# Kernel tuning notes

Hardware: AMD Instinct MI355X
Metric: run time of the kernel (lower is better)

Reference implementation:

```python
import jax, jax.numpy as jnp
import numpy as np

LN_EPS = 1e-6

def layernorm(x, scale, bias):
    mu = jnp.mean(x, axis=-1, keepdims=True)
    var = jnp.mean(jnp.square(x - mu), axis=-1, keepdims=True)
    return (x - mu) * jax.lax.rsqrt(var + LN_EPS) * scale + bias

def setup_inputs() -> dict:
    key = jax.random.key(0)
    ks = jax.random.split(key, 8)
    B, S, Dm = 2, 2048, 1024
    H, Dh, E, De = 16, 64, 8, 1024
    s = 0.02
    return {
        'x': jax.random.normal(ks[0], (B, S, Dm), jnp.float32),
        'ln1_scale': jnp.ones((Dm,), jnp.float32),
        'ln1_bias': jnp.zeros((Dm,), jnp.float32),
        'Wqkv': jax.random.normal(ks[1], (Dm, 3 * H * Dh), jnp.float32) * s,
        'bqkv': jnp.zeros((3 * H * Dh,), jnp.float32),
        'Wo': jax.random.normal(ks[2], (H * Dh, Dm), jnp.float32) * s,
        'bo': jnp.zeros((Dm,), jnp.float32),
        'ln2_scale': jnp.ones((Dm,), jnp.float32),
        'ln2_bias': jnp.zeros((Dm,), jnp.float32),
        'router_W': jax.random.normal(ks[3], (Dm, E), jnp.float32) * s,
        'We': jax.random.normal(ks[4], (E, Dm, De), jnp.float32) * s,
        'be': jnp.zeros((E, De), jnp.float32),
        'Wmo': jax.random.normal(ks[5], (De, Dm), jnp.float32) * s,
        'bmo': jnp.zeros((Dm,), jnp.float32),
    }

def reference(x, ln1_scale, ln1_bias, Wqkv, bqkv, Wo, bo,
              ln2_scale, ln2_bias, router_W, We, be, Wmo, bmo):
    B, S, Dm = x.shape
    H, Dh = 16, 64
    # ---- attention sublayer ----
    y = layernorm(x, ln1_scale, ln1_bias)
    qkv = (y @ Wqkv + bqkv).reshape(B, S, 3, H, Dh)
    qkv = jnp.transpose(qkv, (2, 0, 3, 1, 4))  # [3,B,H,S,Dh]
    q, k, v = qkv[0], qkv[1], qkv[2]
    scale = 1.0 / jnp.sqrt(jnp.float32(Dh))
    attn = jax.nn.softmax(jnp.einsum('bhsd,bhtd->bhst', q, k) * scale, axis=-1)
    o = jnp.einsum('bhst,bhtd->bhsd', attn, v)
    o = jnp.transpose(o, (0, 2, 1, 3)).reshape(B, S, H * Dh)
    x = x + (o @ Wo + bo)
    # ---- dense soft-MoE sublayer ----
    y = layernorm(x, ln2_scale, ln2_bias)
    routing = jax.nn.softmax(jnp.einsum('bsh,he->bse', y, router_W), axis=-1)
    expert_out = jnp.einsum('bsh,ehf->bsef', y, We) + be  # [B,S,E,De]
    combined = jnp.einsum('bse,bsef->bsf', routing, expert_out)
    x = x + (combined @ Wmo + bmo)
    return x
```

## Files before the change

### kernel.cpp

```cpp
#include <hip/hip_runtime.h>
#include <hip/hip_bf16.h>

typedef unsigned short u16;
typedef float f32x4 __attribute__((ext_vector_type(4)));
typedef short s16x8 __attribute__((ext_vector_type(8)));
typedef unsigned short u16x4 __attribute__((ext_vector_type(4)));
typedef unsigned short u16x8 __attribute__((ext_vector_type(8)));

#define T_TOK 4096
#define DM 1024
#define NQKV 3072
#define LN_EPS 1e-6f
#define KDIM 1024
#define NT 32

__device__ __forceinline__ void gll16(const void* g, void* l) {
    __builtin_amdgcn_global_load_lds(
        (const __attribute__((address_space(1))) void*)g,
        (__attribute__((address_space(3))) void*)l, 16, 0, 0);
}

__device__ __forceinline__ void xcd_swz(int& bx, int& by) {
    const int gx = gridDim.x, gy = gridDim.y;
    const int nwg = gx * gy;
    const int lin = by * gx + bx;
    const int cpx = nwg >> 3;
    const int swz = (lin & 7) * cpx + (lin >> 3);
    bx = swz % gx;
    by = swz / gx;
}

__device__ __forceinline__ void bf16_split(float x, u16& hi, u16& lo) {
    unsigned xb = __float_as_uint(x);
    unsigned rh = xb + 0x7fffu + ((xb >> 16) & 1u);
    hi = (u16)(rh >> 16);
    float hf = __uint_as_float(((unsigned)hi) << 16);
    float rs = x - hf;
    unsigned rb = __float_as_uint(rs);
    unsigned rl = rb + 0x7fffu + ((rb >> 16) & 1u);
    lo = (u16)(rl >> 16);
}
__device__ __forceinline__ float bf16_comb(u16 h, u16 l) {
    return __uint_as_float(((unsigned)h) << 16) + __uint_as_float(((unsigned)l) << 16);
}

#define MFMA3(ACC, AH, AL, BH, BL) { \
    ACC = __builtin_amdgcn_mfma_f32_16x16x32_bf16(AH, BH, ACC, 0, 0, 0); \
    ACC = __builtin_amdgcn_mfma_f32_16x16x32_bf16(AH, BL, ACC, 0, 0, 0); \
    ACC = __builtin_amdgcn_mfma_f32_16x16x32_bf16(AL, BH, ACC, 0, 0, 0); }

__global__ __launch_bounds__(256)
void convert_w(const float* __restrict__ src, u16* __restrict__ dh,
               u16* __restrict__ dl, int K, int N) {
    const int e = blockIdx.z;
    src += (size_t)e * K * N;
    dh  += (size_t)e * K * N;
    dl  += (size_t)e * K * N;
    __shared__ float ts[64][65];
    const int t = threadIdx.x;
    const int k0 = blockIdx.y * 64, n0 = blockIdx.x * 64;
    const int r = t >> 4, c4 = (t & 15) * 4;
    #pragma unroll
    for (int i = 0; i < 4; ++i) {
        const int kr = r + i * 16;
        float4 v = *(const float4*)(src + (size_t)(k0 + kr) * N + n0 + c4);
        ts[kr][c4 + 0] = v.x; ts[kr][c4 + 1] = v.y;
        ts[kr][c4 + 2] = v.z; ts[kr][c4 + 3] = v.w;
    }
    __syncthreads();
    #pragma unroll
    for (int i = 0; i < 4; ++i) {
        const int nr = r + i * 16;
        u16x4 h4, l4;
        #pragma unroll
        for (int j = 0; j < 4; ++j) {
            u16 h, l; bf16_split(ts[c4 + j][nr], h, l);
            h4[j] = h; l4[j] = l;
        }
        *(u16x4*)(dh + (size_t)(n0 + nr) * K + k0 + c4) = h4;
        *(u16x4*)(dl + (size_t)(n0 + nr) * K + k0 + c4) = l4;
    }
}

__global__ __launch_bounds__(256)
void ln_kernel(const float* __restrict__ x, const float* __restrict__ sc,
               const float* __restrict__ bi, u16* __restrict__ yh,
               u16* __restrict__ yl) {
    const int row = blockIdx.x;
    const int t = threadIdx.x;
    const float* xr = x + (size_t)row * DM;
    float4 v = *(const float4*)(xr + t * 4);
    float s  = v.x + v.y + v.z + v.w;
    float s2 = v.x*v.x + v.y*v.y + v.z*v.z + v.w*v.w;
    #pragma unroll
    for (int off = 32; off; off >>= 1) {
        s  += __shfl_down(s, off);
        s2 += __shfl_down(s2, off);
    }
    __shared__ float ss[4], ss2[4];
    const int wid = t >> 6;
    if ((t & 63) == 0) { ss[wid] = s; ss2[wid] = s2; }
    __syncthreads();
    const float tot  = ss[0] + ss[1] + ss[2] + ss[3];
    const float tot2 = ss2[0] + ss2[1] + ss2[2] + ss2[3];
    const float mu  = tot * (1.0f / DM);
    const float var = tot2 * (1.0f / DM) - mu * mu;
    const float rcp = rsqrtf(var + LN_EPS);
    float4 sv = *(const float4*)(sc + t * 4);
    float4 bv = *(const float4*)(bi + t * 4);
    float o[4];
    o[0] = (v.x - mu) * rcp * sv.x + bv.x;
    o[1] = (v.y - mu) * rcp * sv.y + bv.y;
    o[2] = (v.z - mu) * rcp * sv.z + bv.z;
    o[3] = (v.w - mu) * rcp * sv.w + bv.w;
    u16x4 h4, l4;
    #pragma unroll
    for (int j = 0; j < 4; ++j) { u16 h, l; bf16_split(o[j], h, l); h4[j] = h; l4[j] = l; }
    *(u16x4*)(yh + (size_t)row * DM + t * 4) = h4;
    *(u16x4*)(yl + (size_t)row * DM + t * 4) = l4;
}

__global__ __launch_bounds__(256, 2)
void qkv_gemm(const u16* __restrict__ Ah, const u16* __restrict__ Al,
              const u16* __restrict__ Bh, const u16* __restrict__ Bl,
              const float* __restrict__ bias,
              u16* __restrict__ qh, u16* __restrict__ ql,
              u16* __restrict__ kh, u16* __restrict__ kl,
              u16* __restrict__ vh, u16* __restrict__ vl) {
    __shared__ __align__(16) u16 Ahs[128 * 32], Als[128 * 32];
    __shared__ __align__(16) u16 Bhs[128 * 32], Bls[128 * 32];
    int bx = blockIdx.x, by = blockIdx.y;
    xcd_swz(bx, by);
    const int t = threadIdx.x;
    const int m0 = by * 128, n0 = bx * 128;
    const int lane = t & 63, wid = t >> 6;
    const int wm = wid >> 1, wn = wid & 1;
    const int lr = lane & 15, lc = lane >> 4;
    const int srow = lane >> 2, skk = (lane & 3) * 8;
    const int w32 = wid * 32;
    const u16* Agh = Ah + (size_t)(m0 + w32 + srow) * KDIM + skk;
    const u16* Agl = Al + (size_t)(m0 + w32 + srow) * KDIM + skk;
    const u16* Bgh = Bh + (size_t)(n0 + w32 + srow) * KDIM + skk;
    const u16* Bgl = Bl + (size_t)(n0 + w32 + srow) * KDIM + skk;

    f32x4 acc[4][4];
    #pragma unroll
    for (int i = 0; i < 4; ++i)
        #pragma unroll
        for (int j = 0; j < 4; ++j)
            #pragma unroll
            for (int r = 0; r < 4; ++r) acc[i][j][r] = 0.0f;

    for (int kt = 0; kt < NT; ++kt) {
        const int ko = kt * 32;
        gll16(Agh + ko,              &Ahs[w32 * 32]);
        gll16(Agh + ko + 16 * KDIM,  &Ahs[(w32 + 16) * 32]);
        gll16(Agl + ko,              &Als[w32 * 32]);
        gll16(Agl + ko + 16 * KDIM,  &Als[(w32 + 16) * 32]);
        gll16(Bgh + ko,              &Bhs[w32 * 32]);
        gll16(Bgh + ko + 16 * KDIM,  &Bhs[(w32 + 16) * 32]);
        gll16(Bgl + ko,              &Bls[w32 * 32]);
        gll16(Bgl + ko + 16 * KDIM,  &Bls[(w32 + 16) * 32]);
        __syncthreads();
        s16x8 fa_h[4], fa_l[4], fb_h[4], fb_l[4];
        #pragma unroll
        for (int fi = 0; fi < 4; ++fi) {
            const int ro = (wm * 64 + fi * 16 + lr) * 32 + lc * 8;
            fa_h[fi] = *(const s16x8*)&Ahs[ro];
            fa_l[fi] = *(const s16x8*)&Als[ro];
        }
        #pragma unroll
        for (int fj = 0; fj < 4; ++fj) {
            const int ro = (wn * 64 + fj * 16 + lr) * 32 + lc * 8;
            fb_h[fj] = *(const s16x8*)&Bhs[ro];
            fb_l[fj] = *(const s16x8*)&Bls[ro];
        }
        #pragma unroll
        for (int fi = 0; fi < 4; ++fi)
            #pragma unroll
            for (int fj = 0; fj < 4; ++fj)
                MFMA3(acc[fi][fj], fa_h[fi], fa_l[fi], fb_h[fj], fb_l[fj])
        __syncthreads();
    }

    #pragma unroll
    for (int fj = 0; fj < 4; ++fj) {
        const int col = n0 + wn * 64 + fj * 16 + lr;
        const int sec = col >> 10;
        const int hh = (col & 1023) >> 6;
        const int dd = col & 63;
        const float bv = bias[col];
        u16* ph = (sec == 0) ? qh : (sec == 1) ? kh : vh;
        u16* pl = (sec == 0) ? ql : (sec == 1) ? kl : vl;
        #pragma unroll
        for (int fi = 0; fi < 4; ++fi)
            #pragma unroll
            for (int r = 0; r < 4; ++r) {
                const int row = m0 + wm * 64 + fi * 16 + lc * 4 + r;
                const int b = row >> 11, s = row & 2047;
                const size_t idx = ((size_t)(b * 16 + hh) * 2048 + s) * 64 + dd;
                u16 h, l; bf16_split(acc[fi][fj][r] + bv, h, l);
                ph[idx] = h; pl[idx] = l;
            }
    }
}

__global__ __launch_bounds__(256, 2)
void gemm_mfma(const u16* __restrict__ Ah, const u16* __restrict__ Al,
               const u16* __restrict__ Bh, const u16* __restrict__ Bl,
               const float* __restrict__ bias, const float* __restrict__ res,
               float* __restrict__ C, int N) {
    __shared__ __align__(16) u16 Ahs[128 * 32], Als[128 * 32];
    __shared__ __align__(16) u16 Bhs[128 * 32], Bls[128 * 32];
    int bx = blockIdx.x, by = blockIdx.y;
    xcd_swz(bx, by);
    const int t = threadIdx.x;
    const int m0 = by * 128, n0 = bx * 128;
    const int lane = t & 63, wid = t >> 6;
    const int wm = wid >> 1, wn = wid & 1;
    const int lr = lane & 15, lc = lane >> 4;
    const int srow = lane >> 2, skk = (lane & 3) * 8;
    const int w32 = wid * 32;
    const u16* Agh = Ah + (size_t)(m0 + w32 + srow) * KDIM + skk;
    const u16* Agl = Al + (size_t)(m0 + w32 + srow) * KDIM + skk;
    const u16* Bgh = Bh + (size_t)(n0 + w32 + srow) * KDIM + skk;
    const u16* Bgl = Bl + (size_t)(n0 + w32 + srow) * KDIM + skk;

    f32x4 acc[4][4];
    #pragma unroll
    for (int i = 0; i < 4; ++i)
        #pragma unroll
        for (int j = 0; j < 4; ++j)
            #pragma unroll
            for (int r = 0; r < 4; ++r) acc[i][j][r] = 0.0f;

    for (int kt = 0; kt < NT; ++kt) {
        const int ko = kt * 32;
        gll16(Agh + ko,              &Ahs[w32 * 32]);
        gll16(Agh + ko + 16 * KDIM,  &Ahs[(w32 + 16) * 32]);
        gll16(Agl + ko,              &Als[w32 * 32]);
        gll16(Agl + ko + 16 * KDIM,  &Als[(w32 + 16) * 32]);
        gll16(Bgh + ko,              &Bhs[w32 * 32]);
        gll16(Bgh + ko + 16 * KDIM,  &Bhs[(w32 + 16) * 32]);
        gll16(Bgl + ko,              &Bls[w32 * 32]);
        gll16(Bgl + ko + 16 * KDIM,  &Bls[(w32 + 16) * 32]);
        __syncthreads();
        s16x8 fa_h[4], fa_l[4], fb_h[4], fb_l[4];
        #pragma unroll
        for (int fi = 0; fi < 4; ++fi) {
            const int ro = (wm * 64 + fi * 16 + lr) * 32 + lc * 8;
            fa_h[fi] = *(const s16x8*)&Ahs[ro];
            fa_l[fi] = *(const s16x8*)&Als[ro];
        }
        #pragma unroll
        for (int fj = 0; fj < 4; ++fj) {
            const int ro = (wn * 64 + fj * 16 + lr) * 32 + lc * 8;
            fb_h[fj] = *(const s16x8*)&Bhs[ro];
            fb_l[fj] = *(const s16x8*)&Bls[ro];
        }
        #pragma unroll
        for (int fi = 0; fi < 4; ++fi)
            #pragma unroll
            for (int fj = 0; fj < 4; ++fj)
                MFMA3(acc[fi][fj], fa_h[fi], fa_l[fi], fb_h[fj], fb_l[fj])
        __syncthreads();
    }

    #pragma unroll
    for (int fj = 0; fj < 4; ++fj) {
        const int col = n0 + wn * 64 + fj * 16 + lr;
        const float bv = bias[col];
        #pragma unroll
        for (int fi = 0; fi < 4; ++fi)
            #pragma unroll
            for (int r = 0; r < 4; ++r) {
                const int row = m0 + wm * 64 + fi * 16 + lc * 4 + r;
                float v = acc[fi][fj][r] + bv + res[(size_t)row * N + col];
                C[(size_t)row * N + col] = v;
            }
    }
}

__global__ __launch_bounds__(256, 2)
void moe_gemm(const u16* __restrict__ Ah, const u16* __restrict__ Al,
              const u16* __restrict__ Bh, const u16* __restrict__ Bl,
              const float* __restrict__ be, const float* __restrict__ gate,
              u16* __restrict__ Ch, u16* __restrict__ Cl) {
    __shared__ __align__(16) u16 Ahs[128 * 32], Als[128 * 32];
    __shared__ __align__(16) u16 Bhs[64 * 32],  Bls[64 * 32];
    int bx = blockIdx.x, by = blockIdx.y;
    xcd_swz(bx, by);
    const int t = threadIdx.x;
    const int m0 = by * 128, n0 = bx * 64;
    const int lane = t & 63, wid = t >> 6;
    const int wm = wid >> 1, wn = wid & 1;
    const int lr = lane & 15, lc = lane >> 4;
    const int srow = lane >> 2, skk = (lane & 3) * 8;
    const int w32 = wid * 32, w16 = wid * 16;
    const u16* Agh = Ah + (size_t)(m0 + w32 + srow) * KDIM + skk;
    const u16* Agl = Al + (size_t)(m0 + w32 + srow) * KDIM + skk;

    f32x4 out[4][2];
    #pragma unroll
    for (int i = 0; i < 4; ++i)
        #pragma unroll
        for (int j = 0; j < 2; ++j)
            #pragma unroll
            for (int r = 0; r < 4; ++r) out[i][j][r] = 0.0f;

    for (int e = 0; e < 8; ++e) {
        const u16* Bgh = Bh + ((size_t)e << 20) + (size_t)(n0 + w16 + srow) * KDIM + skk;
        const u16* Bgl = Bl + ((size_t)e << 20) + (size_t)(n0 + w16 + srow) * KDIM + skk;
        f32x4 acc[4][2];
        #pragma unroll
        for (int i = 0; i < 4; ++i)
            #pragma unroll
            for (int j = 0; j < 2; ++j)
                #pragma unroll
                for (int r = 0; r < 4; ++r) acc[i][j][r] = 0.0f;

        for (int kt = 0; kt < NT; ++kt) {
            const int ko = kt * 32;
            gll16(Agh + ko,             &Ahs[w32 * 32]);
            gll16(Agh + ko + 16 * KDIM, &Ahs[(w32 + 16) * 32]);
            gll16(Agl + ko,             &Als[w32 * 32]);
            gll16(Agl + ko + 16 * KDIM, &Als[(w32 + 16) * 32]);
            gll16(Bgh + ko,             &Bhs[w16 * 32]);
            gll16(Bgl + ko,             &Bls[w16 * 32]);
            __syncthreads();
            s16x8 fa_h[4], fa_l[4], fb_h[2], fb_l[2];
            #pragma unroll
            for (int fi = 0; fi < 4; ++fi) {
                const int ro = (wm * 64 + fi * 16 + lr) * 32 + lc * 8;
                fa_h[fi] = *(const s16x8*)&Ahs[ro];
                fa_l[fi] = *(const s16x8*)&Als[ro];
            }
            #pragma unroll
            for (int fj = 0; fj < 2; ++fj) {
                const int ro = (wn * 32 + fj * 16 + lr) * 32 + lc * 8;
                fb_h[fj] = *(const s16x8*)&Bhs[ro];
                fb_l[fj] = *(const s16x8*)&Bls[ro];
            }
            #pragma unroll
            for (int fi = 0; fi < 4; ++fi)
                #pragma unroll
                for (int fj = 0; fj < 2; ++fj)
                    MFMA3(acc[fi][fj], fa_h[fi], fa_l[fi], fb_h[fj], fb_l[fj])
            __syncthreads();
        }
        float bv[2];
        #pragma unroll
        for (int fj = 0; fj < 2; ++fj)
            bv[fj] = be[e * 1024 + n0 + wn * 32 + fj * 16 + lr];
        #pragma unroll
        for (int fi = 0; fi < 4; ++fi)
            #pragma unroll
            for (int r = 0; r < 4; ++r) {
                const int row = m0 + wm * 64 + fi * 16 + lc * 4 + r;
                const float g = gate[(size_t)row * 8 + e];
                #pragma unroll
                for (int fj = 0; fj < 2; ++fj)
                    out[fi][fj][r] += g * (acc[fi][fj][r] + bv[fj]);
            }
    }
    #pragma unroll
    for (int fi = 0; fi < 4; ++fi)
        #pragma unroll
        for (int fj = 0; fj < 2; ++fj) {
            const int col = n0 + wn * 32 + fj * 16 + lr;
            #pragma unroll
            for (int r = 0; r < 4; ++r) {
                const int row = m0 + wm * 64 + fi * 16 + lc * 4 + r;
                u16 h, l; bf16_split(out[fi][fj][r], h, l);
                Ch[(size_t)row * 1024 + col] = h;
                Cl[(size_t)row * 1024 + col] = l;
            }
        }
}

#define VTS 72
__global__ __launch_bounds__(256, 3)
void attn_kernel(const u16* __restrict__ qh, const u16* __restrict__ ql,
                 const u16* __restrict__ kh, const u16* __restrict__ kl,
                 const u16* __restrict__ vh, const u16* __restrict__ vl,
                 u16* __restrict__ oh, u16* __restrict__ ol) {
    __shared__ __align__(16) u16 Khs[64 * 64], Kls[64 * 64];
    __shared__ __align__(16) u16 Vth[64 * VTS], Vtl[64 * VTS];
    __shared__ __align__(16) u16 Phs[4 * 16 * VTS], Pls[4 * 16 * VTS];
    const int t = threadIdx.x;
    const int lane = t & 63, w = t >> 6;
    const int lr = lane & 15, lc = lane >> 4;
    const int q0 = blockIdx.x * 64;
    const int bh = blockIdx.y;
    const int b = bh >> 4, h = bh & 15;
    const size_t head = (size_t)bh * 2048 * 64;

    s16x8 qf_h[2], qf_l[2];
    {
        const size_t qrow = head + (size_t)(q0 + w * 16 + lr) * 64;
        #pragma unroll
        for (int c = 0; c < 2; ++c) {
            qf_h[c] = *(const s16x8*)(qh + qrow + c * 32 + lc * 8);
            qf_l[c] = *(const s16x8*)(ql + qrow + c * 32 + lc * 8);
        }
    }

    f32x4 o4[4];
    #pragma unroll
    for (int dt = 0; dt < 4; ++dt)
        #pragma unroll
        for (int r = 0; r < 4; ++r) o4[dt][r] = 0.0f;
    float m_run[4], l_run[4];
    #pragma unroll
    for (int r = 0; r < 4; ++r) { m_run[r] = -3.0e38f; l_run[r] = 0.0f; }

    char* const kbase_h = (char*)Khs;
    char* const kbase_l = (char*)Kls;
    u16* const pmy_h = Phs + w * 16 * VTS;
    u16* const pmy_l = Pls + w * 16 * VTS;

    for (int kt = 0; kt < 32; ++kt) {
        __syncthreads();
        {
            const size_t grow = head + (size_t)(kt * 64 + lane) * 64;
            const int dbase = (w & 1) * 32;
            const u16* ksrc = ((w >> 1) ? kl : kh) + grow + dbase;
            char* kdst = (w >> 1) ? kbase_l : kbase_h;
            #pragma unroll
            for (int jj = 0; jj < 4; ++jj) {
                u16x8 kv = *(const u16x8*)(ksrc + jj * 8);
                const int off = (lane * 128 + dbase * 2 + jj * 16) ^ ((lane & 7) << 4);
                *(u16x8*)(kdst + off) = kv;
            }
            const u16* vsrc = ((w >> 1) ? vl : vh) + grow + dbase;
            u16* vdst = (w >> 1) ? Vtl : Vth;
            #pragma unroll
            for (int jj = 0; jj < 4; ++jj) {
                u16x8 vv = *(const u16x8*)(vsrc + jj * 8);
                #pragma unroll
                for (int i = 0; i < 8; ++i)
                    vdst[(dbase + jj * 8 + i) * VTS + lane] = vv[i];
            }
        }
        __syncthreads();

        f32x4 s4[4];
        const int kxor = (lr & 7) << 4;
        #pragma unroll
        for (int j = 0; j < 4; ++j) {
            #pragma unroll
            for (int r = 0; r < 4; ++r) s4[j][r] = 0.0f;
            #pragma unroll
            for (int c = 0; c < 2; ++c) {
                const int off = ((j * 16 + lr) * 128 + c * 64 + lc * 16) ^ kxor;
                s16x8 kb_h = *(const s16x8*)(kbase_h + off);
                s16x8 kb_l = *(const s16x8*)(kbase_l + off);
                MFMA3(s4[j], qf_h[c], qf_l[c], kb_h, kb_l)
            }
        }
        #pragma unroll
        for (int j = 0; j < 4; ++j)
            #pragma unroll
            for (int r = 0; r < 4; ++r) s4[j][r] *= 0.125f;
        #pragma unroll
        for (int r = 0; r < 4; ++r) {
            float tm = fmaxf(fmaxf(s4[0][r], s4[1][r]), fmaxf(s4[2][r], s4[3][r]));
            tm = fmaxf(tm, __shfl_xor(tm, 1));
            tm = fmaxf(tm, __shfl_xor(tm, 2));
            tm = fmaxf(tm, __shfl_xor(tm, 4));
            tm = fmaxf(tm, __shfl_xor(tm, 8));
            const float mn = fmaxf(m_run[r], tm);
            const float corr = __expf(m_run[r] - mn);
            m_run[r] = mn;
            float ps = 0.0f;
            #pragma unroll
            for (int j = 0; j < 4; ++j) {
                const float p = __expf(s4[j][r] - mn);
                s4[j][r] = p;
                ps += p;
            }
            ps += __shfl_xor(ps, 1);
            ps += __shfl_xor(ps, 2);
            ps += __shfl_xor(ps, 4);
            ps += __shfl_xor(ps, 8);
            l_run[r] = l_run[r] * corr + ps;
            #pragma unroll
            for (int dt = 0; dt < 4; ++dt) o4[dt][r] *= corr;
        }
        #pragma unroll
        for (int j = 0; j < 4; ++j)
            #pragma unroll
            for (int r = 0; r < 4; ++r) {
                u16 ph, pl; bf16_split(s4[j][r], ph, pl);
                const int pidx = (lc * 4 + r) * VTS + j * 16 + lr;
                pmy_h[pidx] = ph;
                pmy_l[pidx] = pl;
            }
        #pragma unroll
        for (int kc = 0; kc < 2; ++kc) {
            const int pbase = lr * VTS + kc * 32 + lc * 8;
            s16x8 pa_h = *(const s16x8*)(pmy_h + pbase);
            s16x8 pa_l = *(const s16x8*)(pmy_l + pbase);
            #pragma unroll
            for (int dt = 0; dt < 4; ++dt) {
                const int vbase = (dt * 16 + lr) * VTS + kc * 32 + lc * 8;
                s16x8 vb_h = *(const s16x8*)(Vth + vbase);
                s16x8 vb_l = *(const s16x8*)(Vtl + vbase);
                MFMA3(o4[dt], pa_h, pa_l, vb_h, vb_l)
            }
        }
    }

    float inv[4];
    #pragma unroll
    for (int r = 0; r < 4; ++r) inv[r] = 1.0f / l_run[r];
    #pragma unroll
    for (int dt = 0; dt < 4; ++dt)
        #pragma unroll
        for (int r = 0; r < 4; ++r) {
            const int tok = b * 2048 + q0 + w * 16 + lc * 4 + r;
            const size_t idx = (size_t)tok * 1024 + h * 64 + dt * 16 + lr;
            u16 hh, ll; bf16_split(o4[dt][r] * inv[r], hh, ll);
            oh[idx] = hh; ol[idx] = ll;
        }
}

__global__ __launch_bounds__(64)
void router_kernel(const u16* __restrict__ yh, const u16* __restrict__ yl,
                   const float* __restrict__ rw, float* __restrict__ r) {
    const int tok = blockIdx.x;
    const int lane = threadIdx.x;
    const u16* yhr = yh + (size_t)tok * DM;
    const u16* ylr = yl + (size_t)tok * DM;
    float acc[8] = {0, 0, 0, 0, 0, 0, 0, 0};
    #pragma unroll
    for (int i = 0; i < 16; ++i) {
        const int hh = i * 64 + lane;
        const float yv = bf16_comb(yhr[hh], ylr[hh]);
        const float4 w0 = *(const float4*)(rw + hh * 8);
        const float4 w1 = *(const float4*)(rw + hh * 8 + 4);
        acc[0] = fmaf(yv, w0.x, acc[0]); acc[1] = fmaf(yv, w0.y, acc[1]);
        acc[2] = fmaf(yv, w0.z, acc[2]); acc[3] = fmaf(yv, w0.w, acc[3]);
        acc[4] = fmaf(yv, w1.x, acc[4]); acc[5] = fmaf(yv, w1.y, acc[5]);
        acc[6] = fmaf(yv, w1.z, acc[6]); acc[7] = fmaf(yv, w1.w, acc[7]);
    }
    #pragma unroll
    for (int off = 32; off; off >>= 1)
        #pragma unroll
        for (int e = 0; e < 8; ++e) acc[e] += __shfl_down(acc[e], off);
    if (lane == 0) {
        float mx = acc[0];
        #pragma unroll
        for (int e = 1; e < 8; ++e) mx = fmaxf(mx, acc[e]);
        float p[8], sum = 0.0f;
        #pragma unroll
        for (int e = 0; e < 8; ++e) { p[e] = __expf(acc[e] - mx); sum += p[e]; }
        const float inv = 1.0f / sum;
        #pragma unroll
        for (int e = 0; e < 8; ++e) r[(size_t)tok * 8 + e] = p[e] * inv;
    }
}

extern "C" void kernel_launch(void* const* d_in, const int* in_sizes, int n_in,
                              void* d_out, int out_size, void* d_ws, size_t ws_size,
                              hipStream_t stream) {
    const float* x    = (const float*)d_in[0];
    const float* ln1s = (const float*)d_in[1];
    const float* ln1b = (const float*)d_in[2];
    const float* Wqkv = (const float*)d_in[3];
    const float* bqkv = (const float*)d_in[4];
    const float* Wo   = (const float*)d_in[5];
    const float* bo   = (const float*)d_in[6];
    const float* ln2s = (const float*)d_in[7];
    const float* ln2b = (const float*)d_in[8];
    const float* rW   = (const float*)d_in[9];
    const float* We   = (const float*)d_in[10];
    const float* be   = (const float*)d_in[11];
    const float* Wmo  = (const float*)d_in[12];
    const float* bmo  = (const float*)d_in[13];
    float* out = (float*)d_out;

    char* w = (char*)d_ws;
    auto carve = [&](size_t bytes) {
        void* p = (void*)w;
        w += (bytes + 255) & ~(size_t)255;
        return p;
    };
    const size_t PL = (size_t)T_TOK * DM;
    u16* qh = (u16*)carve(PL * 2); u16* ql = (u16*)carve(PL * 2);
    u16* kh = (u16*)carve(PL * 2); u16* kl = (u16*)carve(PL * 2);
    u16* vh = (u16*)carve(PL * 2); u16* vl = (u16*)carve(PL * 2);
    float* x1  = (float*)carve(PL * 4);
    u16* y_h  = (u16*)carve(PL * 2); u16* y_l  = (u16*)carve(PL * 2);
    u16* ob_h = (u16*)carve(PL * 2); u16* ob_l = (u16*)carve(PL * 2);
    float* r  = (float*)carve((size_t)T_TOK * 8 * 4);
    u16* Wqkv_h = (u16*)carve((size_t)DM * NQKV * 2);
    u16* Wqkv_l = (u16*)carve((size_t)DM * NQKV * 2);
    u16* Wo_h   = (u16*)carve((size_t)DM * DM * 2);
    u16* Wo_l   = (u16*)carve((size_t)DM * DM * 2);
    u16* We_h   = (u16*)carve((size_t)8 * DM * DM * 2);
    u16* We_l   = (u16*)carve((size_t)8 * DM * DM * 2);
    u16* Wmo_h  = (u16*)carve((size_t)DM * DM * 2);
    u16* Wmo_l  = (u16*)carve((size_t)DM * DM * 2);
    u16* cb_h = qh;
    u16* cb_l = ql;

    convert_w<<<dim3(NQKV / 64, DM / 64, 1), 256, 0, stream>>>(Wqkv, Wqkv_h, Wqkv_l, DM, NQKV);
    convert_w<<<dim3(DM / 64, DM / 64, 1), 256, 0, stream>>>(Wo, Wo_h, Wo_l, DM, DM);
    convert_w<<<dim3(DM / 64, DM / 64, 8), 256, 0, stream>>>(We, We_h, We_l, DM, DM);
    convert_w<<<dim3(DM / 64, DM / 64, 1), 256, 0, stream>>>(Wmo, Wmo_h, Wmo_l, DM, DM);

    ln_kernel<<<T_TOK, 256, 0, stream>>>(x, ln1s, ln1b, y_h, y_l);
    qkv_gemm<<<dim3(NQKV / 128, T_TOK / 128), 256, 0, stream>>>(
        y_h, y_l, Wqkv_h, Wqkv_l, bqkv, qh, ql, kh, kl, vh, vl);
    attn_kernel<<<dim3(32, 32), 256, 0, stream>>>(qh, ql, kh, kl, vh, vl, ob_h, ob_l);
    gemm_mfma<<<dim3(DM / 128, T_TOK / 128), 256, 0, stream>>>(
        ob_h, ob_l, Wo_h, Wo_l, bo, x, x1, DM);
    ln_kernel<<<T_TOK, 256, 0, stream>>>(x1, ln2s, ln2b, y_h, y_l);
    router_kernel<<<T_TOK, 64, 0, stream>>>(y_h, y_l, rW, r);
    moe_gemm<<<dim3(DM / 64, T_TOK / 128), 256, 0, stream>>>(
        y_h, y_l, We_h, We_l, be, r, cb_h, cb_l);
    gemm_mfma<<<dim3(DM / 128, T_TOK / 128), 256, 0, stream>>>(
        cb_h, cb_l, Wmo_h, Wmo_l, bmo, x1, out, DM);
}
```

Measured before the change: 887.5 us.

## Run MoE experts as one wide GEMM with a separate combine kernel; prefetch attention K/V

The per-expert MoE loop (128x64 tiles, gating in registers) is replaced by a single 128x128-tile GEMM over all 8 experts at once (N=8192). It writes bias-added expert outputs as single bf16 values. A new combine kernel then takes the routing-weighted sum and splits the result into hi/lo bf16. The aim is a better MFMA tile shape and less repeated A-tile loading, at the cost of a large intermediate buffer written and read through memory, and of lower precision in the expert outputs. The attention kernel also loads the next K/V tile into registers while the current tile is computed, to hide global load latency.

```diff
diff --git a/kernel.cpp b/kernel.cpp
--- a/kernel.cpp
+++ b/kernel.cpp
@@ -39,6 +39,10 @@
     unsigned rb = __float_as_uint(rs);
     unsigned rl = rb + 0x7fffu + ((rb >> 16) & 1u);
     lo = (u16)(rl >> 16);
+}
+__device__ __forceinline__ u16 f2bf(float x) {
+    unsigned xb = __float_as_uint(x);
+    return (u16)((xb + 0x7fffu + ((xb >> 16) & 1u)) >> 16);
 }
 __device__ __forceinline__ float bf16_comb(u16 h, u16 l) {
     return __uint_as_float(((unsigned)h) << 16) + __uint_as_float(((unsigned)l) << 16);
@@ -205,11 +209,12 @@
     }
 }
 
+template<int MODE>
 __global__ __launch_bounds__(256, 2)
 void gemm_mfma(const u16* __restrict__ Ah, const u16* __restrict__ Al,
                const u16* __restrict__ Bh, const u16* __restrict__ Bl,
                const float* __restrict__ bias, const float* __restrict__ res,
-               float* __restrict__ C, int N) {
+               float* __restrict__ C, u16* __restrict__ Cb, int N) {
     __shared__ __align__(16) u16 Ahs[128 * 32], Als[128 * 32];
     __shared__ __align__(16) u16 Bhs[128 * 32], Bls[128 * 32];
     int bx = blockIdx.x, by = blockIdx.y;
@@ -275,107 +280,39 @@
             #pragma unroll
             for (int r = 0; r < 4; ++r) {
                 const int row = m0 + wm * 64 + fi * 16 + lc * 4 + r;
-                float v = acc[fi][fj][r] + bv + res[(size_t)row * N + col];
-                C[(size_t)row * N + col] = v;
-            }
-    }
-}
-
-__global__ __launch_bounds__(256, 2)
-void moe_gemm(const u16* __restrict__ Ah, const u16* __restrict__ Al,
-              const u16* __restrict__ Bh, const u16* __restrict__ Bl,
-              const float* __restrict__ be, const float* __restrict__ gate,
-              u16* __restrict__ Ch, u16* __restrict__ Cl) {
-    __shared__ __align__(16) u16 Ahs[128 * 32], Als[128 * 32];
-    __shared__ __align__(16) u16 Bhs[64 * 32],  Bls[64 * 32];
-    int bx = blockIdx.x, by = blockIdx.y;
-    xcd_swz(bx, by);
-    const int t = threadIdx.x;
-    const int m0 = by * 128, n0 = bx * 64;
-    const int lane = t & 63, wid = t >> 6;
-    const int wm = wid >> 1, wn = wid & 1;
-    const int lr = lane & 15, lc = lane >> 4;
-    const int srow = lane >> 2, skk = (lane & 3) * 8;
-    const int w32 = wid * 32, w16 = wid * 16;
-    const u16* Agh = Ah + (size_t)(m0 + w32 + srow) * KDIM + skk;
-    const u16* Agl = Al + (size_t)(m0 + w32 + srow) * KDIM + skk;
-
-    f32x4 out[4][2];
-    #pragma unroll
-    for (int i = 0; i < 4; ++i)
-        #pragma unroll
-        for (int j = 0; j < 2; ++j)
-            #pragma unroll
-            for (int r = 0; r < 4; ++r) out[i][j][r] = 0.0f;
-
+                if (MODE == 0) {
+                    C[(size_t)row * N + col] =
+                        acc[fi][fj][r] + bv + res[(size_t)row * N + col];
+                } else {
+                    Cb[(size_t)row * N + col] = f2bf(acc[fi][fj][r] + bv);
+                }
+            }
+    }
+}
+
+__global__ __launch_bounds__(256)
+void combine_kernel(const u16* __restrict__ eo, const float* __restrict__ r,
+                    u16* __restrict__ ch, u16* __restrict__ cl) {
+    const int t = blockIdx.x;
+    const int f0 = threadIdx.x * 4;
+    const float* rt = r + (size_t)t * 8;
+    float rr[8];
+    #pragma unroll
+    for (int e = 0; e < 8; ++e) rr[e] = rt[e];
+    const u16* row = eo + (size_t)t * 8192;
+    float acc[4] = {0.0f, 0.0f, 0.0f, 0.0f};
+    #pragma unroll
     for (int e = 0; e < 8; ++e) {
-        const u16* Bgh = Bh + ((size_t)e << 20) + (size_t)(n0 + w16 + srow) * KDIM + skk;
-        const u16* Bgl = Bl + ((size_t)e << 20) + (size_t)(n0 + w16 + srow) * KDIM + skk;
-        f32x4 acc[4][2];
-        #pragma unroll
-        for (int i = 0; i < 4; ++i)
-            #pragma unroll
-            for (int j = 0; j < 2; ++j)
-                #pragma unroll
-                for (int r = 0; r < 4; ++r) acc[i][j][r] = 0.0f;
-
-        for (int kt = 0; kt < NT; ++kt) {
-            const int ko = kt * 32;
-            gll16(Agh + ko,             &Ahs[w32 * 32]);
-            gll16(Agh + ko + 16 * KDIM, &Ahs[(w32 + 16) * 32]);
-            gll16(Agl + ko,             &Als[w32 * 32]);
-            gll16(Agl + ko + 16 * KDIM, &Als[(w32 + 16) * 32]);
-            gll16(Bgh + ko,             &Bhs[w16 * 32]);
-            gll16(Bgl + ko,             &Bls[w16 * 32]);
-            __syncthreads();
-            s16x8 fa_h[4], fa_l[4], fb_h[2], fb_l[2];
-            #pragma unroll
-            for (int fi = 0; fi < 4; ++fi) {
-                const int ro = (wm * 64 + fi * 16 + lr) * 32 + lc * 8;
-                fa_h[fi] = *(const s16x8*)&Ahs[ro];
-                fa_l[fi] = *(const s16x8*)&Als[ro];
-            }
-            #pragma unroll
-            for (int fj = 0; fj < 2; ++fj) {
-                const int ro = (wn * 32 + fj * 16 + lr) * 32 + lc * 8;
-                fb_h[fj] = *(const s16x8*)&Bhs[ro];
-                fb_l[fj] = *(const s16x8*)&Bls[ro];
-            }
-            #pragma unroll
-            for (int fi = 0; fi < 4; ++fi)
-                #pragma unroll
-                for (int fj = 0; fj < 2; ++fj)
-                    MFMA3(acc[fi][fj], fa_h[fi], fa_l[fi], fb_h[fj], fb_l[fj])
-            __syncthreads();
-        }
-        float bv[2];
-        #pragma unroll
-        for (int fj = 0; fj < 2; ++fj)
-            bv[fj] = be[e * 1024 + n0 + wn * 32 + fj * 16 + lr];
-        #pragma unroll
-        for (int fi = 0; fi < 4; ++fi)
-            #pragma unroll
-            for (int r = 0; r < 4; ++r) {
-                const int row = m0 + wm * 64 + fi * 16 + lc * 4 + r;
-                const float g = gate[(size_t)row * 8 + e];
-                #pragma unroll
-                for (int fj = 0; fj < 2; ++fj)
-                    out[fi][fj][r] += g * (acc[fi][fj][r] + bv[fj]);
-            }
-    }
-    #pragma unroll
-    for (int fi = 0; fi < 4; ++fi)
-        #pragma unroll
-        for (int fj = 0; fj < 2; ++fj) {
-            const int col = n0 + wn * 32 + fj * 16 + lr;
-            #pragma unroll
-            for (int r = 0; r < 4; ++r) {
-                const int row = m0 + wm * 64 + fi * 16 + lc * 4 + r;
-                u16 h, l; bf16_split(out[fi][fj][r], h, l);
-                Ch[(size_t)row * 1024 + col] = h;
-                Cl[(size_t)row * 1024 + col] = l;
-            }
-        }
+        u16x4 v = *(const u16x4*)(row + e * 1024 + f0);
+        #pragma unroll
+        for (int j = 0; j < 4; ++j)
+            acc[j] += rr[e] * __uint_as_float(((unsigned)v[j]) << 16);
+    }
+    u16x4 h4, l4;
+    #pragma unroll
+    for (int j = 0; j < 4; ++j) { u16 h, l; bf16_split(acc[j], h, l); h4[j] = h; l4[j] = l; }
+    *(u16x4*)(ch + (size_t)t * 1024 + f0) = h4;
+    *(u16x4*)(cl + (size_t)t * 1024 + f0) = l4;
 }
 
 #define VTS 72
@@ -419,27 +356,38 @@
     u16* const pmy_h = Phs + w * 16 * VTS;
     u16* const pmy_l = Pls + w * 16 * VTS;
 
+    const int dbase = (w & 1) * 32;
+    const u16* kplane = (w >> 1) ? kl : kh;
+    const u16* vplane = (w >> 1) ? vl : vh;
+    char* const kdst = (w >> 1) ? kbase_l : kbase_h;
+    u16* const vdst = (w >> 1) ? Vtl : Vth;
+
+    u16x8 kreg[4], vreg[4];
+    {
+        const size_t grow = head + (size_t)(0 * 64 + lane) * 64 + dbase;
+        #pragma unroll
+        for (int jj = 0; jj < 4; ++jj) {
+            kreg[jj] = *(const u16x8*)(kplane + grow + jj * 8);
+            vreg[jj] = *(const u16x8*)(vplane + grow + jj * 8);
+        }
+    }
+
     for (int kt = 0; kt < 32; ++kt) {
         __syncthreads();
-        {
-            const size_t grow = head + (size_t)(kt * 64 + lane) * 64;
-            const int dbase = (w & 1) * 32;
-            const u16* ksrc = ((w >> 1) ? kl : kh) + grow + dbase;
-            char* kdst = (w >> 1) ? kbase_l : kbase_h;
+        #pragma unroll
+        for (int jj = 0; jj < 4; ++jj) {
+            const int off = (lane * 128 + dbase * 2 + jj * 16) ^ ((lane & 7) << 4);
+            *(u16x8*)(kdst + off) = kreg[jj];
+            #pragma unroll
+            for (int i = 0; i < 8; ++i)
+                vdst[(dbase + jj * 8 + i) * VTS + lane] = vreg[jj][i];
+        }
+        if (kt + 1 < 32) {
+            const size_t grow = head + (size_t)((kt + 1) * 64 + lane) * 64 + dbase;
             #pragma unroll
             for (int jj = 0; jj < 4; ++jj) {
-                u16x8 kv = *(const u16x8*)(ksrc + jj * 8);
-                const int off = (lane * 128 + dbase * 2 + jj * 16) ^ ((lane & 7) << 4);
-                *(u16x8*)(kdst + off) = kv;
-            }
-            const u16* vsrc = ((w >> 1) ? vl : vh) + grow + dbase;
-            u16* vdst = (w >> 1) ? Vtl : Vth;
-            #pragma unroll
-            for (int jj = 0; jj < 4; ++jj) {
-                u16x8 vv = *(const u16x8*)(vsrc + jj * 8);
-                #pragma unroll
-                for (int i = 0; i < 8; ++i)
-                    vdst[(dbase + jj * 8 + i) * VTS + lane] = vv[i];
+                kreg[jj] = *(const u16x8*)(kplane + grow + jj * 8);
+                vreg[jj] = *(const u16x8*)(vplane + grow + jj * 8);
             }
         }
         __syncthreads();
@@ -590,9 +538,9 @@
     u16* qh = (u16*)carve(PL * 2); u16* ql = (u16*)carve(PL * 2);
     u16* kh = (u16*)carve(PL * 2); u16* kl = (u16*)carve(PL * 2);
     u16* vh = (u16*)carve(PL * 2); u16* vl = (u16*)carve(PL * 2);
+    u16* ob_h = (u16*)carve(PL * 2); u16* ob_l = (u16*)carve(PL * 2);
     float* x1  = (float*)carve(PL * 4);
     u16* y_h  = (u16*)carve(PL * 2); u16* y_l  = (u16*)carve(PL * 2);
-    u16* ob_h = (u16*)carve(PL * 2); u16* ob_l = (u16*)carve(PL * 2);
     float* r  = (float*)carve((size_t)T_TOK * 8 * 4);
     u16* Wqkv_h = (u16*)carve((size_t)DM * NQKV * 2);
     u16* Wqkv_l = (u16*)carve((size_t)DM * NQKV * 2);
@@ -602,8 +550,9 @@
     u16* We_l   = (u16*)carve((size_t)8 * DM * DM * 2);
     u16* Wmo_h  = (u16*)carve((size_t)DM * DM * 2);
     u16* Wmo_l  = (u16*)carve((size_t)DM * DM * 2);
-    u16* cb_h = qh;
-    u16* cb_l = ql;
+    u16* eo = qh;
+    u16* cb_h = y_h;
+    u16* cb_l = y_l;
 
     convert_w<<<dim3(NQKV / 64, DM / 64, 1), 256, 0, stream>>>(Wqkv, Wqkv_h, Wqkv_l, DM, NQKV);
     convert_w<<<dim3(DM / 64, DM / 64, 1), 256, 0, stream>>>(Wo, Wo_h, Wo_l, DM, DM);
@@ -614,12 +563,13 @@
     qkv_gemm<<<dim3(NQKV / 128, T_TOK / 128), 256, 0, stream>>>(
         y_h, y_l, Wqkv_h, Wqkv_l, bqkv, qh, ql, kh, kl, vh, vl);
     attn_kernel<<<dim3(32, 32), 256, 0, stream>>>(qh, ql, kh, kl, vh, vl, ob_h, ob_l);
-    gemm_mfma<<<dim3(DM / 128, T_TOK / 128), 256, 0, stream>>>(
-        ob_h, ob_l, Wo_h, Wo_l, bo, x, x1, DM);
+    gemm_mfma<0><<<dim3(DM / 128, T_TOK / 128), 256, 0, stream>>>(
+        ob_h, ob_l, Wo_h, Wo_l, bo, x, x1, nullptr, DM);
     ln_kernel<<<T_TOK, 256, 0, stream>>>(x1, ln2s, ln2b, y_h, y_l);
     router_kernel<<<T_TOK, 64, 0, stream>>>(y_h, y_l, rW, r);
-    moe_gemm<<<dim3(DM / 64, T_TOK / 128), 256, 0, stream>>>(
-        y_h, y_l, We_h, We_l, be, r, cb_h, cb_l);
-    gemm_mfma<<<dim3(DM / 128, T_TOK / 128), 256, 0, stream>>>(
-        cb_h, cb_l, Wmo_h, Wmo_l, bmo, x1, out, DM);
-}
+    gemm_mfma<1><<<dim3(8192 / 128, T_TOK / 128), 256, 0, stream>>>(
+        y_h, y_l, We_h, We_l, be, nullptr, nullptr, eo, 8192);
+    combine_kernel<<<T_TOK, 256, 0, stream>>>(eo, r, cb_h, cb_l);
+    gemm_mfma<0><<<dim3(DM / 128, T_TOK / 128), 256, 0, stream>>>(
+        cb_h, cb_l, Wmo_h, Wmo_l, bmo, x1, out, nullptr, DM);
+}
```

Result: faster. 824.7 us (-7.1%).
